# Kernel optimization log

Hardware: AMD Instinct MI355X
Metric: run time of the kernel (lower is better)

## Reference

```python
import jax, jax.numpy as jnp
import numpy as np

N, E, P = 50000, 800000, 500000
NODE_IN, HIDDEN, EDGE_IN = 128, 256, 16


def setup_inputs() -> dict:
    key = jax.random.key(0)
    ks = jax.random.split(key, 16)
    s = lambda k, shape, fan_in: jax.random.normal(k, shape, jnp.float32) * (1.0 / np.sqrt(fan_in))
    return {
        "x": jax.random.normal(ks[0], (N, NODE_IN), jnp.float32),
        "edge_index": jax.random.randint(ks[1], (2, E), 0, N),
        "edge_u": jax.random.randint(ks[2], (P,), 0, N),
        "edge_v": jax.random.randint(ks[3], (P,), 0, N),
        "edge_attr": jax.random.normal(ks[4], (P, EDGE_IN), jnp.float32),
        "log_exposure": jax.random.normal(ks[5], (P,), jnp.float32),
        # conv1: lin_l (on mean-aggregated neighbors, with bias), lin_r (on root, no bias)
        "Wl1": s(ks[6], (HIDDEN, NODE_IN), NODE_IN),
        "bl1": jnp.zeros((HIDDEN,), jnp.float32),
        "Wr1": s(ks[7], (HIDDEN, NODE_IN), NODE_IN),
        # conv2
        "Wl2": s(ks[8], (HIDDEN, HIDDEN), HIDDEN),
        "bl2": jnp.zeros((HIDDEN,), jnp.float32),
        "Wr2": s(ks[9], (HIDDEN, HIDDEN), HIDDEN),
        # edge MLP: Linear(2*hidden+edge_in, hidden) -> ReLU -> Linear(hidden, 1)
        "W1": s(ks[10], (HIDDEN, 2 * HIDDEN + EDGE_IN), 2 * HIDDEN + EDGE_IN),
        "b1": jnp.zeros((HIDDEN,), jnp.float32),
        "W2": s(ks[11], (1, HIDDEN), HIDDEN),
        "b2": jnp.zeros((1,), jnp.float32),
    }


def sage_conv(x, src, dst, Wl, bl, Wr):
    # PyG SAGEConv, mean aggregation: out = lin_l(mean_{j in N(i)} x_j) + lin_r(x_i)
    n = x.shape[0]
    agg = jax.ops.segment_sum(x[src], dst, num_segments=n)          # [N, F]
    cnt = jax.ops.segment_sum(jnp.ones((src.shape[0],), x.dtype), dst, num_segments=n)
    agg = agg / jnp.maximum(cnt, 1.0)[:, None]
    return agg @ Wl.T + bl + x @ Wr.T


def reference(x, edge_index, edge_u, edge_v, edge_attr, log_exposure,
              Wl1, bl1, Wr1, Wl2, bl2, Wr2, W1, b1, W2, b2):
    src, dst = edge_index[0], edge_index[1]
    # eval mode: dropout is identity
    h = jax.nn.relu(sage_conv(x, src, dst, Wl1, bl1, Wr1))
    h = jax.nn.relu(sage_conv(h, src, dst, Wl2, bl2, Wr2))
    z = jnp.concatenate([h[edge_u], h[edge_v], edge_attr], axis=1)  # [P, 2H+Ein]
    s = (jax.nn.relu(z @ W1.T + b1) @ W2.T + b2)[:, 0]              # [P]
    return log_exposure + s
```

## Files before the change

### kernel.cpp

```cpp
#include <hip/hip_runtime.h>


typedef float f32x4 __attribute__((ext_vector_type(4)));
typedef __bf16 bf16x8 __attribute__((ext_vector_type(8)));

__device__ __forceinline__ unsigned short f2b(float f) {
    unsigned u = __float_as_uint(f);
    u = u + 0x7fffu + ((u >> 16) & 1u);
    return (unsigned short)(u >> 16);
}
__device__ __forceinline__ float b2f(unsigned short s) {
    return __uint_as_float(((unsigned)s) << 16);
}
__device__ __forceinline__ float blo(unsigned x) { return b2f((unsigned short)(x & 0xffffu)); }
__device__ __forceinline__ float bhi(unsigned x) { return b2f((unsigned short)(x >> 16)); }
__device__ __forceinline__ unsigned packsum(unsigned a, unsigned b) {
    return (unsigned)f2b(blo(a) + blo(b)) | ((unsigned)f2b(bhi(a) + bhi(b)) << 16);
}
__device__ __forceinline__ int swz(int r, int g) { return (g + (r >> 1)) & 3; }


__global__ void k_count(const int* __restrict__ dst, int* __restrict__ cnt, int E) {
    int e = blockIdx.x * 256 + threadIdx.x;
    if (e < E) atomicAdd(&cnt[dst[e]], 1);
}

__global__ __launch_bounds__(1024) void k_scan(int* __restrict__ cnt_cursor,
                                               int* __restrict__ row_ptr, int n) {
    __shared__ int wsum[16];
    __shared__ int carry;
    int t = threadIdx.x, lane = t & 63, w = t >> 6;
    if (t == 0) carry = 0;
    __syncthreads();
    int nch = (n + 1023) >> 10;
    for (int ch = 0; ch < nch; ++ch) {
        int i = (ch << 10) + t;
        int v = (i < n) ? cnt_cursor[i] : 0;
        int s = v;
        #pragma unroll
        for (int off = 1; off < 64; off <<= 1) {
            int u = __shfl_up(s, off);
            if (lane >= off) s += u;
        }
        if (lane == 63) wsum[w] = s;
        __syncthreads();
        int wpre = 0;
        for (int j = 0; j < w; ++j) wpre += wsum[j];
        int incl = s + wpre;
        int base = carry;
        if (i < n) { int ex = base + incl - v; row_ptr[i] = ex; cnt_cursor[i] = ex; }
        __syncthreads();
        if (t == 1023) carry = base + incl;
    }
    __syncthreads();
    if (t == 0) row_ptr[n] = carry;
}

__global__ void k_scatter(const int* __restrict__ src, const int* __restrict__ dst,
                          int* __restrict__ cursor, int* __restrict__ bucket, int E) {
    int e = blockIdx.x * 256 + threadIdx.x;
    if (e < E) {
        int p = atomicAdd(&cursor[dst[e]], 1);
        bucket[p] = src[e];
    }
}


__global__ void k_convert_weights(const float* __restrict__ Wl1, const float* __restrict__ Wr1,
                                  const float* __restrict__ Wl2, const float* __restrict__ Wr2,
                                  const float* __restrict__ W1, const float* __restrict__ b1,
                                  unsigned short* __restrict__ Wc1,
                                  unsigned short* __restrict__ Wc2,
                                  unsigned short* __restrict__ W1g,
                                  unsigned short* __restrict__ WaF) {
    int idx = blockIdx.x * 256 + threadIdx.x;
    if (idx < 65536) {
        int c = idx >> 13, j = (idx >> 5) & 255, kk = idx & 31;
        float v = (c < 4) ? Wl1[j * 128 + c * 32 + kk] : Wr1[j * 128 + (c - 4) * 32 + kk];
        Wc1[idx] = f2b(v);
    } else if (idx < 65536 + 131072) {
        int i2 = idx - 65536;
        int c = i2 >> 13, j = (i2 >> 5) & 255, kk = i2 & 31;
        float v = (c < 8) ? Wl2[j * 256 + c * 32 + kk] : Wr2[j * 256 + (c - 8) * 32 + kk];
        Wc2[i2] = f2b(v);
    } else if (idx < 65536 + 131072 + 131072) {
        int i3 = idx - 65536 - 131072;
        int c = i3 >> 14, j = (i3 >> 5) & 511, kk = i3 & 31;
        float v = (j < 256) ? W1[(size_t)j * 528 + c * 32 + kk]
                            : W1[(size_t)(j - 256) * 528 + 256 + c * 32 + kk];
        W1g[i3] = f2b(v);
    } else if (idx < 65536 + 131072 + 131072 + 8192) {
        int i4 = idx - 65536 - 131072 - 131072;
        int mi = i4 >> 9, l = (i4 >> 3) & 63, j = i4 & 7;
        int m = mi * 16 + (l & 15);
        int k = (l >> 4) * 8 + j;
        float v = (k < 16) ? W1[(size_t)m * 528 + 512 + k] : (k == 16 ? b1[m] : 0.f);
        WaF[i4] = f2b(v);
    }
}

__global__ void k_f2b_copy(const float* __restrict__ in, unsigned short* __restrict__ out, int n) {
    int i = blockIdx.x * 256 + threadIdx.x;
    if (i < n) out[i] = f2b(in[i]);
}


__device__ __forceinline__ void acc8(uint4 v, float* s) {
    s[0] += blo(v.x); s[1] += bhi(v.x);
    s[2] += blo(v.y); s[3] += bhi(v.y);
    s[4] += blo(v.z); s[5] += bhi(v.z);
    s[6] += blo(v.w); s[7] += bhi(v.w);
}

__global__ __launch_bounds__(256) void k_agg_x(const unsigned short* __restrict__ xb,
                                               const int* __restrict__ row_ptr,
                                               const int* __restrict__ bucket,
                                               unsigned short* __restrict__ agg, int Nn) {
    int node = blockIdx.x * 4 + (threadIdx.x >> 6);
    if (node >= Nn) return;
    int lane = threadIdx.x & 63;
    int q = lane >> 4, c = lane & 15;
    int beg = row_ptr[node], end = row_ptr[node + 1];
    int len = end - beg;
    int lo = beg + ((len * q) >> 2);
    int hi = beg + ((len * (q + 1)) >> 2);
    float s[8] = {0.f,0.f,0.f,0.f,0.f,0.f,0.f,0.f};
    const unsigned short* xp = xb + c * 8;
    int e = lo;
    for (; e + 4 <= hi; e += 4) {
        int b0 = bucket[e], b1 = bucket[e + 1], b2 = bucket[e + 2], b3 = bucket[e + 3];
        uint4 v0 = *reinterpret_cast<const uint4*>(xp + (size_t)b0 * 128);
        uint4 v1 = *reinterpret_cast<const uint4*>(xp + (size_t)b1 * 128);
        uint4 v2 = *reinterpret_cast<const uint4*>(xp + (size_t)b2 * 128);
        uint4 v3 = *reinterpret_cast<const uint4*>(xp + (size_t)b3 * 128);
        acc8(v0, s); acc8(v1, s); acc8(v2, s); acc8(v3, s);
    }
    for (; e < hi; ++e)
        acc8(*reinterpret_cast<const uint4*>(xp + (size_t)bucket[e] * 128), s);
    #pragma unroll
    for (int j = 0; j < 8; ++j) {
        s[j] += __shfl_xor(s[j], 16);
        s[j] += __shfl_xor(s[j], 32);
    }
    if (q == 0) {
        float sc = 1.0f / (float)(len > 1 ? len : 1);
        uint4 o;
        o.x = (unsigned)f2b(s[0]*sc) | ((unsigned)f2b(s[1]*sc) << 16);
        o.y = (unsigned)f2b(s[2]*sc) | ((unsigned)f2b(s[3]*sc) << 16);
        o.z = (unsigned)f2b(s[4]*sc) | ((unsigned)f2b(s[5]*sc) << 16);
        o.w = (unsigned)f2b(s[6]*sc) | ((unsigned)f2b(s[7]*sc) << 16);
        *reinterpret_cast<uint4*>(agg + (size_t)node * 128 + c * 8) = o;
    }
}

__global__ __launch_bounds__(256) void k_agg_h(const unsigned short* __restrict__ h,
                                               const int* __restrict__ row_ptr,
                                               const int* __restrict__ bucket,
                                               unsigned short* __restrict__ agg, int Nn) {
    int node = blockIdx.x * 4 + (threadIdx.x >> 6);
    if (node >= Nn) return;
    int lane = threadIdx.x & 63;
    int g = lane >> 5, c = lane & 31;
    int beg = row_ptr[node], end = row_ptr[node + 1];
    int len = end - beg;
    int lo = beg + ((len * g) >> 1);
    int hi = beg + ((len * (g + 1)) >> 1);
    float s[8] = {0.f,0.f,0.f,0.f,0.f,0.f,0.f,0.f};
    const unsigned short* hp = h + c * 8;
    int e = lo;
    for (; e + 4 <= hi; e += 4) {
        int b0 = bucket[e], b1 = bucket[e + 1], b2 = bucket[e + 2], b3 = bucket[e + 3];
        uint4 v0 = *reinterpret_cast<const uint4*>(hp + (size_t)b0 * 256);
        uint4 v1 = *reinterpret_cast<const uint4*>(hp + (size_t)b1 * 256);
        uint4 v2 = *reinterpret_cast<const uint4*>(hp + (size_t)b2 * 256);
        uint4 v3 = *reinterpret_cast<const uint4*>(hp + (size_t)b3 * 256);
        acc8(v0, s); acc8(v1, s); acc8(v2, s); acc8(v3, s);
    }
    for (; e < hi; ++e)
        acc8(*reinterpret_cast<const uint4*>(hp + (size_t)bucket[e] * 256), s);
    #pragma unroll
    for (int j = 0; j < 8; ++j) s[j] += __shfl_xor(s[j], 32);
    if (g == 0) {
        float sc = 1.0f / (float)(len > 1 ? len : 1);
        uint4 o;
        o.x = (unsigned)f2b(s[0]*sc) | ((unsigned)f2b(s[1]*sc) << 16);
        o.y = (unsigned)f2b(s[2]*sc) | ((unsigned)f2b(s[3]*sc) << 16);
        o.z = (unsigned)f2b(s[4]*sc) | ((unsigned)f2b(s[5]*sc) << 16);
        o.w = (unsigned)f2b(s[6]*sc) | ((unsigned)f2b(s[7]*sc) << 16);
        *reinterpret_cast<uint4*>(agg + (size_t)node * 256 + c * 8) = o;
    }
}


__global__ __launch_bounds__(256) void k_conv_gemm(const unsigned short* __restrict__ Aagg,
                                                   const unsigned short* __restrict__ Aself,
                                                   const unsigned short* __restrict__ Wck,
                                                   const float* __restrict__ bias,
                                                   unsigned short* __restrict__ Hout,
                                                   int Nn, int F) {
    __shared__ __align__(16) unsigned short zt[128 * 32];
    __shared__ __align__(16) unsigned short wt[128 * 32];
    const int t = threadIdx.x;
    const int lane = t & 63, w = t >> 6;
    const int wm = w >> 1, wn = w & 1;
    const int node0 = blockIdx.x * 128;
    const int colh = blockIdx.y;
    const int half = F >> 5, nchunks = F >> 4;

    f32x4 acc[4][4];
    #pragma unroll
    for (int i = 0; i < 4; ++i)
        #pragma unroll
        for (int j = 0; j < 4; ++j) acc[i][j] = (f32x4){0.f, 0.f, 0.f, 0.f};

    for (int c = 0; c < nchunks; ++c) {
        __syncthreads();
        const unsigned short* Asrc = (c < half) ? Aagg : Aself;
        const int ccol = ((c < half) ? c : c - half) * 32;
        #pragma unroll
        for (int p = 0; p < 2; ++p) {
            int fc = t + p * 256;
            int row = fc >> 2, seg = fc & 3;
            int node = node0 + row; if (node >= Nn) node = Nn - 1;
            uint4 v = *reinterpret_cast<const uint4*>(Asrc + (size_t)node * F + ccol + seg * 8);
            *reinterpret_cast<uint4*>(&zt[row * 32 + swz(row, seg) * 8]) = v;
        }
        const unsigned short* Wsrc = Wck + ((size_t)c * 256 + colh * 128) * 32;
        #pragma unroll
        for (int p = 0; p < 2; ++p) {
            int fc = t + p * 256;
            int row = fc >> 2, seg = fc & 3;
            *reinterpret_cast<uint4*>(&wt[row * 32 + swz(row, seg) * 8]) =
                *reinterpret_cast<const uint4*>(Wsrc + fc * 8);
        }
        __syncthreads();
        bf16x8 a[4], b[4];
        const int q = lane >> 4;
        #pragma unroll
        for (int mi = 0; mi < 4; ++mi) {
            int R = wm * 64 + mi * 16 + (lane & 15);
            a[mi] = *reinterpret_cast<const bf16x8*>(&zt[R * 32 + swz(R, q) * 8]);
        }
        #pragma unroll
        for (int ni = 0; ni < 4; ++ni) {
            int R = wn * 64 + ni * 16 + (lane & 15);
            b[ni] = *reinterpret_cast<const bf16x8*>(&wt[R * 32 + swz(R, q) * 8]);
        }
        #pragma unroll
        for (int mi = 0; mi < 4; ++mi)
            #pragma unroll
            for (int ni = 0; ni < 4; ++ni)
                acc[mi][ni] = __builtin_amdgcn_mfma_f32_16x16x32_bf16(a[mi], b[ni], acc[mi][ni], 0, 0, 0);
    }

    #pragma unroll
    for (int mi = 0; mi < 4; ++mi)
        #pragma unroll
        for (int ni = 0; ni < 4; ++ni) {
            int col = colh * 128 + wn * 64 + ni * 16 + (lane & 15);
            float bia = bias[col];
            #pragma unroll
            for (int r = 0; r < 4; ++r) {
                int row = node0 + wm * 64 + mi * 16 + ((lane >> 4) << 2) + r;
                if (row < Nn) {
                    float v = acc[mi][ni][r] + bia;
                    v = v > 0.f ? v : 0.f;
                    Hout[(size_t)row * 256 + col] = f2b(v);
                }
            }
        }
}


__global__ __launch_bounds__(256) void k_gemm_g(const unsigned short* __restrict__ A,
                                                const unsigned short* __restrict__ Wck,
                                                unsigned short* __restrict__ Gout,
                                                int Nn) {
    __shared__ __align__(16) unsigned short zt[128 * 32];
    __shared__ __align__(16) unsigned short wt[128 * 32];
    const int t = threadIdx.x;
    const int lane = t & 63, w = t >> 6;
    const int wm = w >> 1, wn = w & 1;
    const int node0 = blockIdx.x * 128;
    const int colg = blockIdx.y;

    f32x4 acc[4][4];
    #pragma unroll
    for (int i = 0; i < 4; ++i)
        #pragma unroll
        for (int j = 0; j < 4; ++j) acc[i][j] = (f32x4){0.f, 0.f, 0.f, 0.f};

    for (int c = 0; c < 8; ++c) {
        __syncthreads();
        #pragma unroll
        for (int p = 0; p < 2; ++p) {
            int fc = t + p * 256;
            int row = fc >> 2, seg = fc & 3;
            int node = node0 + row; if (node >= Nn) node = Nn - 1;
            uint4 v = *reinterpret_cast<const uint4*>(A + (size_t)node * 256 + c * 32 + seg * 8);
            *reinterpret_cast<uint4*>(&zt[row * 32 + swz(row, seg) * 8]) = v;
        }
        const unsigned short* Wsrc = Wck + ((size_t)c * 512 + colg * 128) * 32;
        #pragma unroll
        for (int p = 0; p < 2; ++p) {
            int fc = t + p * 256;
            int row = fc >> 2, seg = fc & 3;
            *reinterpret_cast<uint4*>(&wt[row * 32 + swz(row, seg) * 8]) =
                *reinterpret_cast<const uint4*>(Wsrc + fc * 8);
        }
        __syncthreads();
        bf16x8 a[4], b[4];
        const int q = lane >> 4;
        #pragma unroll
        for (int mi = 0; mi < 4; ++mi) {
            int R = wm * 64 + mi * 16 + (lane & 15);
            a[mi] = *reinterpret_cast<const bf16x8*>(&zt[R * 32 + swz(R, q) * 8]);
        }
        #pragma unroll
        for (int ni = 0; ni < 4; ++ni) {
            int R = wn * 64 + ni * 16 + (lane & 15);
            b[ni] = *reinterpret_cast<const bf16x8*>(&wt[R * 32 + swz(R, q) * 8]);
        }
        #pragma unroll
        for (int mi = 0; mi < 4; ++mi)
            #pragma unroll
            for (int ni = 0; ni < 4; ++ni)
                acc[mi][ni] = __builtin_amdgcn_mfma_f32_16x16x32_bf16(a[mi], b[ni], acc[mi][ni], 0, 0, 0);
    }

    #pragma unroll
    for (int mi = 0; mi < 4; ++mi)
        #pragma unroll
        for (int ni = 0; ni < 4; ++ni) {
            int col = colg * 128 + wn * 64 + ni * 16 + (lane & 15);
            #pragma unroll
            for (int r = 0; r < 4; ++r) {
                int row = node0 + wm * 64 + mi * 16 + ((lane >> 4) << 2) + r;
                if (row < Nn)
                    Gout[(size_t)row * 512 + col] = f2b(acc[mi][ni][r]);
            }
        }
}


__global__ __launch_bounds__(256) void k_edge(const unsigned short* __restrict__ G2,
                                              const float* __restrict__ attr,
                                              const int* __restrict__ eu,
                                              const int* __restrict__ ev,
                                              const uint4* __restrict__ WaF,
                                              const float* __restrict__ W2,
                                              const float* __restrict__ b2,
                                              const float* __restrict__ logexp,
                                              float* __restrict__ out, int P) {
    __shared__ __align__(16) unsigned short attrT[64 * 40];
    __shared__ __align__(16) unsigned short gt[64 * 264];
    __shared__ float w2s[256];
    const int t = threadIdx.x;
    const int lane = t & 63, w = t >> 6;
    const int base = blockIdx.x * 64;

    {
        int e = t >> 2, seg = t & 3;
        int eg = base + e; if (eg >= P) eg = P - 1;
        const float4 f = *reinterpret_cast<const float4*>(attr + (size_t)eg * 16 + seg * 4);
        uint2 o;
        o.x = (unsigned)f2b(f.x) | ((unsigned)f2b(f.y) << 16);
        o.y = (unsigned)f2b(f.z) | ((unsigned)f2b(f.w) << 16);
        *reinterpret_cast<uint2*>(&attrT[e * 40 + seg * 4]) = o;
    }
    if (t < 64) {
        uint2 z0; z0.x = 0x3f80u; z0.y = 0u;
        *reinterpret_cast<uint2*>(&attrT[t * 40 + 16]) = z0;
        uint2 z1; z1.x = 0u; z1.y = 0u;
        *reinterpret_cast<uint2*>(&attrT[t * 40 + 20]) = z1;
        uint4 z2; z2.x = z2.y = z2.z = z2.w = 0u;
        *reinterpret_cast<uint4*>(&attrT[t * 40 + 24]) = z2;
    }
    w2s[t] = W2[t];
    __syncthreads();

    {
        const int h = lane >> 5, c = lane & 31;
        #pragma unroll
        for (int i = 0; i < 8; ++i) {
            int el = w * 16 + 2 * i + h;
            int eg = base + el; if (eg >= P) eg = P - 1;
            int u = eu[eg], v = ev[eg];
            uint4 a = *reinterpret_cast<const uint4*>(G2 + (size_t)u * 512 + c * 8);
            uint4 bb = *reinterpret_cast<const uint4*>(G2 + (size_t)v * 512 + 256 + c * 8);
            uint4 o;
            o.x = packsum(a.x, bb.x);
            o.y = packsum(a.y, bb.y);
            o.z = packsum(a.z, bb.z);
            o.w = packsum(a.w, bb.w);
            *reinterpret_cast<uint4*>(&gt[el * 264 + c * 8]) = o;
        }
    }

    const int el = lane & 15, q = lane >> 4;
    const int grow = w * 16 + el;
    const bf16x8 bfrag = *reinterpret_cast<const bf16x8*>(&attrT[grow * 40 + q * 8]);
    float s = 0.f;
    #pragma unroll
    for (int mi = 0; mi < 16; ++mi) {
        const bf16x8 af = *reinterpret_cast<const bf16x8*>(&WaF[mi * 64 + lane]);
        f32x4 acc = __builtin_amdgcn_mfma_f32_16x16x32_bf16(af, bfrag, (f32x4){0.f,0.f,0.f,0.f}, 0, 0, 0);
        const uint2 gv2 = *reinterpret_cast<const uint2*>(&gt[grow * 264 + mi * 16 + q * 4]);
        const float4 w2v = *reinterpret_cast<const float4*>(&w2s[mi * 16 + q * 4]);
        float y0 = acc[0] + blo(gv2.x);
        float y1 = acc[1] + bhi(gv2.x);
        float y2 = acc[2] + blo(gv2.y);
        float y3 = acc[3] + bhi(gv2.y);
        s += (y0 > 0.f ? y0 : 0.f) * w2v.x;
        s += (y1 > 0.f ? y1 : 0.f) * w2v.y;
        s += (y2 > 0.f ? y2 : 0.f) * w2v.z;
        s += (y3 > 0.f ? y3 : 0.f) * w2v.w;
    }
    s += __shfl_xor(s, 16);
    s += __shfl_xor(s, 32);
    int eg = base + grow;
    if (q == 0 && eg < P)
        out[eg] = logexp[eg] + b2[0] + s;
}


extern "C" void kernel_launch(void* const* d_in, const int* in_sizes, int n_in,
                              void* d_out, int out_size, void* d_ws, size_t ws_size,
                              hipStream_t stream) {
    const float* x      = (const float*)d_in[0];
    const int*   eidx   = (const int*)d_in[1];
    const int*   eu     = (const int*)d_in[2];
    const int*   ev     = (const int*)d_in[3];
    const float* attr   = (const float*)d_in[4];
    const float* logexp = (const float*)d_in[5];
    const float* Wl1    = (const float*)d_in[6];
    const float* bl1    = (const float*)d_in[7];
    const float* Wr1    = (const float*)d_in[8];
    const float* Wl2    = (const float*)d_in[9];
    const float* bl2    = (const float*)d_in[10];
    const float* Wr2    = (const float*)d_in[11];
    const float* W1     = (const float*)d_in[12];
    const float* b1     = (const float*)d_in[13];
    const float* W2     = (const float*)d_in[14];
    const float* b2     = (const float*)d_in[15];
    float* out = (float*)d_out;

    const int N = in_sizes[0] / 128;
    const int E = in_sizes[1] / 2;
    const int P = in_sizes[2];
    const int* src = eidx;
    const int* dst = eidx + E;

    char* ws = (char*)d_ws;
    size_t off = 0;
    auto alloc = [&](size_t bytes) -> void* {
        off = (off + 255) & ~(size_t)255;
        void* p = ws + off;
        off += bytes;
        return p;
    };
    int* row_ptr = (int*)alloc((size_t)(N + 1) * 4);
    int* cursor  = (int*)alloc((size_t)N * 4);
    int* bucket  = (int*)alloc((size_t)E * 4);
    unsigned short* h1 = (unsigned short*)alloc((size_t)N * 256 * 2);
    unsigned short* h2 = (unsigned short*)alloc((size_t)N * 256 * 2);
    char* shared_base = (char*)alloc((size_t)N * 512 * 2);
    unsigned short* xb   = (unsigned short*)shared_base;
    unsigned short* agg1 = (unsigned short*)(shared_base + (size_t)N * 128 * 2);
    unsigned short* agg2 = (unsigned short*)(shared_base + (size_t)N * 256 * 2);
    unsigned short* G2   = (unsigned short*)shared_base;
    unsigned short* Wc1  = (unsigned short*)alloc((size_t)65536 * 2);
    unsigned short* Wc2  = (unsigned short*)alloc((size_t)131072 * 2);
    unsigned short* W1g  = (unsigned short*)alloc((size_t)131072 * 2);
    unsigned short* WaF  = (unsigned short*)alloc((size_t)8192 * 2);

    hipMemsetAsync(cursor, 0, (size_t)N * 4, stream);
    k_count<<<(E + 255) / 256, 256, 0, stream>>>(dst, cursor, E);
    k_scan<<<1, 1024, 0, stream>>>(cursor, row_ptr, N);
    k_scatter<<<(E + 255) / 256, 256, 0, stream>>>(src, dst, cursor, bucket, E);
    k_convert_weights<<<(65536 + 131072 + 131072 + 8192 + 255) / 256, 256, 0, stream>>>(
        Wl1, Wr1, Wl2, Wr2, W1, b1, Wc1, Wc2, W1g, WaF);
    k_f2b_copy<<<(N * 128 + 255) / 256, 256, 0, stream>>>(x, xb, N * 128);

    k_agg_x<<<(N + 3) / 4, 256, 0, stream>>>(xb, row_ptr, bucket, agg1, N);
    dim3 gconv((N + 127) / 128, 2);
    k_conv_gemm<<<gconv, 256, 0, stream>>>(agg1, xb, Wc1, bl1, h1, N, 128);
    k_agg_h<<<(N + 3) / 4, 256, 0, stream>>>(h1, row_ptr, bucket, agg2, N);
    k_conv_gemm<<<gconv, 256, 0, stream>>>(agg2, h1, Wc2, bl2, h2, N, 256);

    dim3 gg((N + 127) / 128, 4);
    k_gemm_g<<<gg, 256, 0, stream>>>(h2, W1g, G2, N);
    k_edge<<<(P + 63) / 64, 256, 0, stream>>>(G2, attr, eu, ev, (const uint4*)WaF,
                                              W2, b2, logexp, out, P);
}
```

Baseline: 525.5 us.

## Gather neighbor features in FP8 for mean aggregation; split edge G sums

```diff
diff --git a/kernel.cpp b/kernel.cpp
--- a/kernel.cpp
+++ b/kernel.cpp
@@ -2,6 +2,7 @@
 
 
 typedef float f32x4 __attribute__((ext_vector_type(4)));
+typedef float f32x2 __attribute__((ext_vector_type(2)));
 typedef __bf16 bf16x8 __attribute__((ext_vector_type(8)));
 
 __device__ __forceinline__ unsigned short f2b(float f) {
@@ -14,10 +15,10 @@
 }
 __device__ __forceinline__ float blo(unsigned x) { return b2f((unsigned short)(x & 0xffffu)); }
 __device__ __forceinline__ float bhi(unsigned x) { return b2f((unsigned short)(x >> 16)); }
-__device__ __forceinline__ unsigned packsum(unsigned a, unsigned b) {
-    return (unsigned)f2b(blo(a) + blo(b)) | ((unsigned)f2b(bhi(a) + bhi(b)) << 16);
-}
 __device__ __forceinline__ int swz(int r, int g) { return (g + (r >> 1)) & 3; }
+__device__ __forceinline__ unsigned char f2f8(float v) {
+    return (unsigned char)(__builtin_amdgcn_cvt_pk_fp8_f32(v, v, 0, false) & 0xff);
+}
 
 
 __global__ void k_count(const int* __restrict__ dst, int* __restrict__ cnt, int E) {
@@ -99,20 +100,28 @@
     }
 }
 
-__global__ void k_f2b_copy(const float* __restrict__ in, unsigned short* __restrict__ out, int n) {
-    int i = blockIdx.x * 256 + threadIdx.x;
-    if (i < n) out[i] = f2b(in[i]);
-}
-
-
-__device__ __forceinline__ void acc8(uint4 v, float* s) {
-    s[0] += blo(v.x); s[1] += bhi(v.x);
-    s[2] += blo(v.y); s[3] += bhi(v.y);
-    s[4] += blo(v.z); s[5] += bhi(v.z);
-    s[6] += blo(v.w); s[7] += bhi(v.w);
-}
-
-__global__ __launch_bounds__(256) void k_agg_x(const unsigned short* __restrict__ xb,
+__global__ void k_xconvert(const float* __restrict__ in, unsigned short* __restrict__ xb,
+                           unsigned char* __restrict__ xf8, int n) {
+    int j = (blockIdx.x * 256 + threadIdx.x) * 2;
+    if (j < n) {
+        float a = in[j], b = in[j + 1];
+        xb[j] = f2b(a); xb[j + 1] = f2b(b);
+        unsigned p = __builtin_amdgcn_cvt_pk_fp8_f32(a, b, 0, false);
+        *reinterpret_cast<unsigned short*>(xf8 + j) = (unsigned short)(p & 0xffffu);
+    }
+}
+
+
+__device__ __forceinline__ void accf8(uint2 v, float* s) {
+    f32x2 p0 = __builtin_amdgcn_cvt_pk_f32_fp8(v.x, false);
+    f32x2 p1 = __builtin_amdgcn_cvt_pk_f32_fp8(v.x, true);
+    f32x2 p2 = __builtin_amdgcn_cvt_pk_f32_fp8(v.y, false);
+    f32x2 p3 = __builtin_amdgcn_cvt_pk_f32_fp8(v.y, true);
+    s[0] += p0.x; s[1] += p0.y; s[2] += p1.x; s[3] += p1.y;
+    s[4] += p2.x; s[5] += p2.y; s[6] += p3.x; s[7] += p3.y;
+}
+
+__global__ __launch_bounds__(256) void k_agg_x(const unsigned char* __restrict__ xf8,
                                                const int* __restrict__ row_ptr,
                                                const int* __restrict__ bucket,
                                                unsigned short* __restrict__ agg, int Nn) {
@@ -125,18 +134,18 @@
     int lo = beg + ((len * q) >> 2);
     int hi = beg + ((len * (q + 1)) >> 2);
     float s[8] = {0.f,0.f,0.f,0.f,0.f,0.f,0.f,0.f};
-    const unsigned short* xp = xb + c * 8;
+    const unsigned char* xp = xf8 + c * 8;
     int e = lo;
     for (; e + 4 <= hi; e += 4) {
         int b0 = bucket[e], b1 = bucket[e + 1], b2 = bucket[e + 2], b3 = bucket[e + 3];
-        uint4 v0 = *reinterpret_cast<const uint4*>(xp + (size_t)b0 * 128);
-        uint4 v1 = *reinterpret_cast<const uint4*>(xp + (size_t)b1 * 128);
-        uint4 v2 = *reinterpret_cast<const uint4*>(xp + (size_t)b2 * 128);
-        uint4 v3 = *reinterpret_cast<const uint4*>(xp + (size_t)b3 * 128);
-        acc8(v0, s); acc8(v1, s); acc8(v2, s); acc8(v3, s);
+        uint2 v0 = *reinterpret_cast<const uint2*>(xp + (size_t)b0 * 128);
+        uint2 v1 = *reinterpret_cast<const uint2*>(xp + (size_t)b1 * 128);
+        uint2 v2 = *reinterpret_cast<const uint2*>(xp + (size_t)b2 * 128);
+        uint2 v3 = *reinterpret_cast<const uint2*>(xp + (size_t)b3 * 128);
+        accf8(v0, s); accf8(v1, s); accf8(v2, s); accf8(v3, s);
     }
     for (; e < hi; ++e)
-        acc8(*reinterpret_cast<const uint4*>(xp + (size_t)bucket[e] * 128), s);
+        accf8(*reinterpret_cast<const uint2*>(xp + (size_t)bucket[e] * 128), s);
     #pragma unroll
     for (int j = 0; j < 8; ++j) {
         s[j] += __shfl_xor(s[j], 16);
@@ -153,7 +162,7 @@
     }
 }
 
-__global__ __launch_bounds__(256) void k_agg_h(const unsigned short* __restrict__ h,
+__global__ __launch_bounds__(256) void k_agg_h(const unsigned char* __restrict__ hf8,
                                                const int* __restrict__ row_ptr,
                                                const int* __restrict__ bucket,
                                                unsigned short* __restrict__ agg, int Nn) {
@@ -166,18 +175,18 @@
     int lo = beg + ((len * g) >> 1);
     int hi = beg + ((len * (g + 1)) >> 1);
     float s[8] = {0.f,0.f,0.f,0.f,0.f,0.f,0.f,0.f};
-    const unsigned short* hp = h + c * 8;
+    const unsigned char* hp = hf8 + c * 8;
     int e = lo;
     for (; e + 4 <= hi; e += 4) {
         int b0 = bucket[e], b1 = bucket[e + 1], b2 = bucket[e + 2], b3 = bucket[e + 3];
-        uint4 v0 = *reinterpret_cast<const uint4*>(hp + (size_t)b0 * 256);
-        uint4 v1 = *reinterpret_cast<const uint4*>(hp + (size_t)b1 * 256);
-        uint4 v2 = *reinterpret_cast<const uint4*>(hp + (size_t)b2 * 256);
-        uint4 v3 = *reinterpret_cast<const uint4*>(hp + (size_t)b3 * 256);
-        acc8(v0, s); acc8(v1, s); acc8(v2, s); acc8(v3, s);
+        uint2 v0 = *reinterpret_cast<const uint2*>(hp + (size_t)b0 * 256);
+        uint2 v1 = *reinterpret_cast<const uint2*>(hp + (size_t)b1 * 256);
+        uint2 v2 = *reinterpret_cast<const uint2*>(hp + (size_t)b2 * 256);
+        uint2 v3 = *reinterpret_cast<const uint2*>(hp + (size_t)b3 * 256);
+        accf8(v0, s); accf8(v1, s); accf8(v2, s); accf8(v3, s);
     }
     for (; e < hi; ++e)
-        acc8(*reinterpret_cast<const uint4*>(hp + (size_t)bucket[e] * 256), s);
+        accf8(*reinterpret_cast<const uint2*>(hp + (size_t)bucket[e] * 256), s);
     #pragma unroll
     for (int j = 0; j < 8; ++j) s[j] += __shfl_xor(s[j], 32);
     if (g == 0) {
@@ -197,6 +206,7 @@
                                                    const unsigned short* __restrict__ Wck,
                                                    const float* __restrict__ bias,
                                                    unsigned short* __restrict__ Hout,
+                                                   unsigned char* __restrict__ Hf8,
                                                    int Nn, int F) {
     __shared__ __align__(16) unsigned short zt[128 * 32];
     __shared__ __align__(16) unsigned short wt[128 * 32];
@@ -266,6 +276,7 @@
                     float v = acc[mi][ni][r] + bia;
                     v = v > 0.f ? v : 0.f;
                     Hout[(size_t)row * 256 + col] = f2b(v);
+                    if (Hf8) Hf8[(size_t)row * 256 + col] = f2f8(v);
                 }
             }
         }
@@ -353,7 +364,8 @@
                                               const float* __restrict__ logexp,
                                               float* __restrict__ out, int P) {
     __shared__ __align__(16) unsigned short attrT[64 * 40];
-    __shared__ __align__(16) unsigned short gt[64 * 264];
+    __shared__ __align__(16) unsigned short guT[64 * 264];
+    __shared__ __align__(16) unsigned short gvT[64 * 264];
     __shared__ float w2s[256];
     const int t = threadIdx.x;
     const int lane = t & 63, w = t >> 6;
@@ -388,12 +400,8 @@
             int u = eu[eg], v = ev[eg];
             uint4 a = *reinterpret_cast<const uint4*>(G2 + (size_t)u * 512 + c * 8);
             uint4 bb = *reinterpret_cast<const uint4*>(G2 + (size_t)v * 512 + 256 + c * 8);
-            uint4 o;
-            o.x = packsum(a.x, bb.x);
-            o.y = packsum(a.y, bb.y);
-            o.z = packsum(a.z, bb.z);
-            o.w = packsum(a.w, bb.w);
-            *reinterpret_cast<uint4*>(&gt[el * 264 + c * 8]) = o;
+            *reinterpret_cast<uint4*>(&guT[el * 264 + c * 8]) = a;
+            *reinterpret_cast<uint4*>(&gvT[el * 264 + c * 8]) = bb;
         }
     }
 
@@ -405,12 +413,13 @@
     for (int mi = 0; mi < 16; ++mi) {
         const bf16x8 af = *reinterpret_cast<const bf16x8*>(&WaF[mi * 64 + lane]);
         f32x4 acc = __builtin_amdgcn_mfma_f32_16x16x32_bf16(af, bfrag, (f32x4){0.f,0.f,0.f,0.f}, 0, 0, 0);
-        const uint2 gv2 = *reinterpret_cast<const uint2*>(&gt[grow * 264 + mi * 16 + q * 4]);
+        const uint2 gu2 = *reinterpret_cast<const uint2*>(&guT[grow * 264 + mi * 16 + q * 4]);
+        const uint2 gv2 = *reinterpret_cast<const uint2*>(&gvT[grow * 264 + mi * 16 + q * 4]);
         const float4 w2v = *reinterpret_cast<const float4*>(&w2s[mi * 16 + q * 4]);
-        float y0 = acc[0] + blo(gv2.x);
-        float y1 = acc[1] + bhi(gv2.x);
-        float y2 = acc[2] + blo(gv2.y);
-        float y3 = acc[3] + bhi(gv2.y);
+        float y0 = acc[0] + blo(gu2.x) + blo(gv2.x);
+        float y1 = acc[1] + bhi(gu2.x) + bhi(gv2.x);
+        float y2 = acc[2] + blo(gu2.y) + blo(gv2.y);
+        float y3 = acc[3] + bhi(gu2.y) + bhi(gv2.y);
         s += (y0 > 0.f ? y0 : 0.f) * w2v.x;
         s += (y1 > 0.f ? y1 : 0.f) * w2v.y;
         s += (y2 > 0.f ? y2 : 0.f) * w2v.z;
@@ -469,6 +478,8 @@
     unsigned short* agg1 = (unsigned short*)(shared_base + (size_t)N * 128 * 2);
     unsigned short* agg2 = (unsigned short*)(shared_base + (size_t)N * 256 * 2);
     unsigned short* G2   = (unsigned short*)shared_base;
+    unsigned char* xf8  = (unsigned char*)alloc((size_t)N * 128);
+    unsigned char* h1f8 = (unsigned char*)alloc((size_t)N * 256);
     unsigned short* Wc1  = (unsigned short*)alloc((size_t)65536 * 2);
     unsigned short* Wc2  = (unsigned short*)alloc((size_t)131072 * 2);
     unsigned short* W1g  = (unsigned short*)alloc((size_t)131072 * 2);
@@ -480,13 +491,13 @@
     k_scatter<<<(E + 255) / 256, 256, 0, stream>>>(src, dst, cursor, bucket, E);
     k_convert_weights<<<(65536 + 131072 + 131072 + 8192 + 255) / 256, 256, 0, stream>>>(
         Wl1, Wr1, Wl2, Wr2, W1, b1, Wc1, Wc2, W1g, WaF);
-    k_f2b_copy<<<(N * 128 + 255) / 256, 256, 0, stream>>>(x, xb, N * 128);
-
-    k_agg_x<<<(N + 3) / 4, 256, 0, stream>>>(xb, row_ptr, bucket, agg1, N);
+    k_xconvert<<<(N * 64 + 255) / 256, 256, 0, stream>>>(x, xb, xf8, N * 128);
+
+    k_agg_x<<<(N + 3) / 4, 256, 0, stream>>>(xf8, row_ptr, bucket, agg1, N);
     dim3 gconv((N + 127) / 128, 2);
-    k_conv_gemm<<<gconv, 256, 0, stream>>>(agg1, xb, Wc1, bl1, h1, N, 128);
-    k_agg_h<<<(N + 3) / 4, 256, 0, stream>>>(h1, row_ptr, bucket, agg2, N);
-    k_conv_gemm<<<gconv, 256, 0, stream>>>(agg2, h1, Wc2, bl2, h2, N, 256);
+    k_conv_gemm<<<gconv, 256, 0, stream>>>(agg1, xb, Wc1, bl1, h1, h1f8, N, 128);
+    k_agg_h<<<(N + 3) / 4, 256, 0, stream>>>(h1f8, row_ptr, bucket, agg2, N);
+    k_conv_gemm<<<gconv, 256, 0, stream>>>(agg2, h1, Wc2, bl2, h2, (unsigned char*)nullptr, N, 256);
 
     dim3 gg((N + 127) / 128, 4);
     k_gemm_g<<<gg, 256, 0, stream>>>(h2, W1g, G2, N);
```

Result: no change. 534.5 us (+1.7%).
